# Optimization experiments

Measured on AMD Instinct MI355X. Metric: run time of the kernel, lower is better.

## Reference

```python
import jax, jax.numpy as jnp
import numpy as np

N_NODES = 100000
N_EDGES = 800000
NUM_GRAPHS = 512
IN_DIM = 16
EDGE_DIM = 1
HID = 64       # emb_dim
MLP_H = 32     # hidden_layers inside each MPNNLayer
L = 3          # num_layers
EPS = 1e-5


def setup_inputs() -> dict:
    key = jax.random.key(0)
    ks = jax.random.split(key, 24)
    s = 0.05
    inp = {
        "x": jax.random.normal(ks[0], (N_NODES, IN_DIM), jnp.float32),
        "edge_index": jax.random.randint(ks[1], (2, N_EDGES), 0, N_NODES),
        "edge_attr": jax.random.uniform(ks[2], (N_EDGES, EDGE_DIM), jnp.float32),
        "batch": jnp.sort(jax.random.randint(ks[3], (N_NODES,), 0, NUM_GRAPHS)),
        # input projection
        "lin_in_w": jax.random.normal(ks[4], (IN_DIM, HID), jnp.float32) * s,
        "lin_in_b": jnp.zeros((HID,), jnp.float32),
        # message MLP (stacked over L layers): Linear(129->32), BN(32), ReLU, Linear(32->64), ReLU, BN(64)
        "msg_w1": jax.random.normal(ks[5], (L, 2 * HID + EDGE_DIM, MLP_H), jnp.float32) * s,
        "msg_b1": jnp.zeros((L, MLP_H), jnp.float32),
        "msg_g1": jnp.ones((L, MLP_H), jnp.float32),
        "msg_be1": jnp.zeros((L, MLP_H), jnp.float32),
        "msg_w2": jax.random.normal(ks[6], (L, MLP_H, HID), jnp.float32) * s,
        "msg_b2": jnp.zeros((L, HID), jnp.float32),
        "msg_g2": jnp.ones((L, HID), jnp.float32),
        "msg_be2": jnp.zeros((L, HID), jnp.float32),
        # update MLP: Linear(128->32), BN(32), ReLU, Linear(32->64), ReLU, BN(64)
        "upd_w1": jax.random.normal(ks[7], (L, 2 * HID, MLP_H), jnp.float32) * s,
        "upd_b1": jnp.zeros((L, MLP_H), jnp.float32),
        "upd_g1": jnp.ones((L, MLP_H), jnp.float32),
        "upd_be1": jnp.zeros((L, MLP_H), jnp.float32),
        "upd_w2": jax.random.normal(ks[8], (L, MLP_H, HID), jnp.float32) * s,
        "upd_b2": jnp.zeros((L, HID), jnp.float32),
        "upd_g2": jnp.ones((L, HID), jnp.float32),
        "upd_be2": jnp.zeros((L, HID), jnp.float32),
        # head Linear(64->1) + ReLU
        "out_w": jax.random.normal(ks[9], (HID, 1), jnp.float32) * s,
        "out_b": jnp.zeros((1,), jnp.float32),
    }
    return inp


def _bn(h, g, b):
    # BatchNorm1d, training-mode batch stats (biased variance), dropout treated as identity (eval)
    mu = jnp.mean(h, axis=0)
    var = jnp.var(h, axis=0)
    return g * (h - mu) * jax.lax.rsqrt(var + EPS) + b


def reference(x, edge_index, edge_attr, batch,
              lin_in_w, lin_in_b,
              msg_w1, msg_b1, msg_g1, msg_be1, msg_w2, msg_b2, msg_g2, msg_be2,
              upd_w1, upd_b1, upd_g1, upd_be1, upd_w2, upd_b2, upd_g2, upd_be2,
              out_w, out_b):
    src = edge_index[0]  # x_j source
    dst = edge_index[1]  # x_i target / aggregation index
    h = x @ lin_in_w + lin_in_b  # [N, HID]
    for l in range(L):
        # message: cat([x_i, x_j, edge_attr]) -> Linear -> BN -> ReLU -> Linear -> ReLU -> BN
        m_in = jnp.concatenate([h[dst], h[src], edge_attr], axis=1)  # [E, 2*HID+EDGE_DIM]
        m = jax.nn.relu(_bn(m_in @ msg_w1[l] + msg_b1[l], msg_g1[l], msg_be1[l]))
        m = _bn(jax.nn.relu(m @ msg_w2[l] + msg_b2[l]), msg_g2[l], msg_be2[l])
        # aggregate: scatter-add over destination nodes
        agg = jax.ops.segment_sum(m, dst, num_segments=N_NODES)  # [N, HID]
        # update: cat([x, aggr]) -> Linear -> BN -> ReLU -> Linear -> ReLU -> BN
        u_in = jnp.concatenate([h, agg], axis=1)  # [N, 2*HID]
        u = jax.nn.relu(_bn(u_in @ upd_w1[l] + upd_b1[l], upd_g1[l], upd_be1[l]))
        u = _bn(jax.nn.relu(u @ upd_w2[l] + upd_b2[l]), upd_g2[l], upd_be2[l])
        h = h + u  # residual (x += conv(...))
    # global mean pool
    pooled = jax.ops.segment_sum(h, batch, num_segments=NUM_GRAPHS)
    counts = jax.ops.segment_sum(jnp.ones((h.shape[0],), h.dtype), batch, num_segments=NUM_GRAPHS)
    pooled = pooled / jnp.maximum(counts, 1.0)[:, None]
    return jax.nn.relu(pooled @ out_w + out_b).reshape(-1)  # [NUM_GRAPHS]
```

## Files before the change

kernel.cpp:

```cpp
#include <hip/hip_runtime.h>
#include <hip/hip_bf16.h>

#define N_NODES   100000
#define N_EDGES   800000
#define NUM_GRAPHS 512
#define IN_DIM    16
#define HID       64
#define MLP_H     32
#define EPS       1e-5f
#define TPB       256
#define SCAN_B    1024
#define NCHUNK    ((N_NODES + SCAN_B - 1) / SCAN_B)
#define GSB       2048
#define NWAVES    (GSB * 4)
#define PER_W     ((N_EDGES + NWAVES - 1) / NWAVES)
#define NODEBLKS  ((N_NODES + 63) / 64)

using nh2   = decltype(__builtin_amdgcn_cvt_pkrtz(0.f, 0.f));
typedef _Float16 f16x8 __attribute__((ext_vector_type(8)));
typedef float    f32x4 __attribute__((ext_vector_type(4)));
typedef int      i32x4 __attribute__((ext_vector_type(4)));

__device__ __forceinline__ nh2 pack2(float a, float b) {
  return __builtin_amdgcn_cvt_pkrtz(a, b);
}
__device__ __forceinline__ float wsum(float v) {
  v += __shfl_xor(v, 1, 64);
  v += __shfl_xor(v, 2, 64);
  v += __shfl_xor(v, 4, 64);
  v += __shfl_xor(v, 8, 64);
  v += __shfl_xor(v, 16, 64);
  v += __shfl_xor(v, 32, 64);
  return v;
}
__device__ __forceinline__ int lbound(const int* __restrict__ rs, int key) {
  int lo = 0, hi = N_NODES;
  while (lo < hi) { int m = (lo + hi) >> 1; if (rs[m] < key) lo = m + 1; else hi = m; }
  return lo;
}

__global__ __launch_bounds__(TPB) void k_deg(const int* __restrict__ ei, int* __restrict__ deg) {
  int e = blockIdx.x * TPB + threadIdx.x;
  if (e < N_EDGES) atomicAdd(&deg[ei[N_EDGES + e]], 1);
}

__global__ __launch_bounds__(SCAN_B) void k_scan_part(const int* __restrict__ deg,
                                                      int* __restrict__ partials) {
  __shared__ int red[SCAN_B];
  int i = blockIdx.x * SCAN_B + threadIdx.x;
  red[threadIdx.x] = (i < N_NODES) ? deg[i] : 0;
  __syncthreads();
  for (int off = SCAN_B / 2; off > 0; off >>= 1) {
    if (threadIdx.x < off) red[threadIdx.x] += red[threadIdx.x + off];
    __syncthreads();
  }
  if (threadIdx.x == 0) partials[blockIdx.x] = red[0];
}

__global__ void k_scan_mid(int* __restrict__ partials, int* __restrict__ row_start) {
  int run = 0;
  for (int b = 0; b < NCHUNK; ++b) { int t = partials[b]; partials[b] = run; run += t; }
  row_start[N_NODES] = run;
}

__global__ __launch_bounds__(SCAN_B) void k_scan_fin(const int* __restrict__ deg,
                                                     const int* __restrict__ partials,
                                                     int* __restrict__ row_start,
                                                     int* __restrict__ cursor) {
  __shared__ int buf[2][SCAN_B];
  int t = threadIdx.x, i = blockIdx.x * SCAN_B + t;
  int v = (i < N_NODES) ? deg[i] : 0;
  buf[0][t] = v;
  __syncthreads();
  int cur = 0;
  for (int off = 1; off < SCAN_B; off <<= 1) {
    int nv = buf[cur][t] + ((t >= off) ? buf[cur][t - off] : 0);
    buf[cur ^ 1][t] = nv; cur ^= 1;
    __syncthreads();
  }
  if (i < N_NODES) {
    int excl = buf[cur][t] - v + partials[blockIdx.x];
    row_start[i] = excl;
    cursor[i] = excl;
  }
}

__global__ __launch_bounds__(TPB) void k_fill(const int* __restrict__ ei,
                                              const float* __restrict__ ea,
                                              int* __restrict__ cursor,
                                              i32x4* __restrict__ erec) {
  int e = blockIdx.x * TPB + threadIdx.x;
  if (e >= N_EDGES) return;
  int dst = ei[N_EDGES + e];
  int pos = atomicAdd(&cursor[dst], 1);
  i32x4 rec;
  rec[0] = ei[e];
  rec[1] = dst;
  rec[2] = __float_as_int(ea[e]);
  rec[3] = 0;
  erec[pos] = rec;
}

__global__ __launch_bounds__(TPB) void k_lin_in(const float* __restrict__ x,
                                                const float* __restrict__ w,
                                                const float* __restrict__ b,
                                                float* __restrict__ h) {
  int i = blockIdx.x * TPB + threadIdx.x;
  if (i >= N_NODES) return;
  float xi[IN_DIM];
  const float4* xp = reinterpret_cast<const float4*>(x + i * IN_DIM);
#pragma unroll
  for (int q = 0; q < 4; ++q) {
    float4 v = xp[q];
    xi[4*q] = v.x; xi[4*q+1] = v.y; xi[4*q+2] = v.z; xi[4*q+3] = v.w;
  }
  float4* hp = reinterpret_cast<float4*>(h + i * HID);
#pragma unroll
  for (int j4 = 0; j4 < HID/4; ++j4) {
    float o[4];
#pragma unroll
    for (int c = 0; c < 4; ++c) {
      int j = j4*4 + c;
      float acc = b[j];
#pragma unroll
      for (int k = 0; k < IN_DIM; ++k) acc += xi[k] * w[k*HID + j];
      o[c] = acc;
    }
    float4 ov = {o[0], o[1], o[2], o[3]};
    hp[j4] = ov;
  }
}

__global__ __launch_bounds__(TPB) void k_pq(const float* __restrict__ h,
                                            const float* __restrict__ w1,
                                            const float* __restrict__ b1,
                                            float* __restrict__ P,
                                            _Float16* __restrict__ Qh) {
  const int part = __builtin_amdgcn_readfirstlane(threadIdx.x >> 6);
  const int lane = threadIdx.x & 63;
  const int i = blockIdx.x * 64 + lane;
  if (i >= N_NODES) return;
  const int jb = (part & 1) * 16;
  const bool isQ = part >= 2;
  const float* wbase = w1 + (isQ ? 64 * MLP_H : 0) + jb;
  float acc[16];
#pragma unroll
  for (int j = 0; j < 16; ++j) acc[j] = isQ ? 0.f : b1[jb + j];
  const float4* hp = reinterpret_cast<const float4*>(h + i * HID);
#pragma unroll 4
  for (int k4 = 0; k4 < 16; ++k4) {
    float4 a = hp[k4];
    const float* wr = wbase + (k4*4) * MLP_H;
#pragma unroll
    for (int j = 0; j < 16; ++j)
      acc[j] += a.x*wr[j] + a.y*wr[MLP_H+j] + a.z*wr[2*MLP_H+j] + a.w*wr[3*MLP_H+j];
  }
  if (!isQ) {
    float4* pp = reinterpret_cast<float4*>(P + i * MLP_H + jb);
#pragma unroll
    for (int c = 0; c < 4; ++c) {
      float4 o = {acc[4*c], acc[4*c+1], acc[4*c+2], acc[4*c+3]};
      pp[c] = o;
    }
  } else {
    i32x4 o0, o1;
#pragma unroll
    for (int c = 0; c < 4; ++c) {
      o0[c] = __builtin_bit_cast(int, pack2(acc[2*c],     acc[2*c+1]));
      o1[c] = __builtin_bit_cast(int, pack2(acc[8+2*c],   acc[8+2*c+1]));
    }
    i32x4* qp = reinterpret_cast<i32x4*>(Qh + i * MLP_H + jb);
    qp[0] = o0; qp[1] = o1;
  }
}

__global__ __launch_bounds__(TPB) void k_gather(const float* __restrict__ P,
                                                const _Float16* __restrict__ Qh,
                                                const i32x4* __restrict__ erec,
                                                const float* __restrict__ w1,
                                                float* __restrict__ gstat) {
  const int lane = threadIdx.x & 63;
  const int fg   = lane & 3;
  const int sl   = lane >> 2;
  const int fb   = fg * 8;
  float wk[8];
#pragma unroll
  for (int i = 0; i < 8; ++i) wk[i] = w1[128 * MLP_H + fb + i];
  float sv[8], qs[8];
#pragma unroll
  for (int i = 0; i < 8; ++i) { sv[i] = 0.f; qs[i] = 0.f; }
  const int wv = blockIdx.x * 4 + (threadIdx.x >> 6);
  const int c0 = wv * PER_W;
  const int c1 = min(c0 + PER_W, N_EDGES);
  if (c0 < N_EDGES) {
    const int c1m1 = c1 - 1;
    const int rounds = (c1 - c0 + 15) >> 4;
#define EIDX(R) min(c0 + 16*(R) + sl, c1m1)
    i32x4 recA = erec[EIDX(0)];
    i32x4 recB = erec[EIDX(1)];
    i32x4 recH = erec[EIDX(2)];
    f16x8 qA  = *reinterpret_cast<const f16x8*>(Qh + recA[0] * MLP_H + fb);
    f32x4 pA0 = *reinterpret_cast<const f32x4*>(P + recA[1] * MLP_H + fb);
    f32x4 pA1 = *reinterpret_cast<const f32x4*>(P + recA[1] * MLP_H + fb + 4);
    float aA  = __int_as_float(recA[2]);
    f16x8 qB  = *reinterpret_cast<const f16x8*>(Qh + recB[0] * MLP_H + fb);
    f32x4 pB0 = *reinterpret_cast<const f32x4*>(P + recB[1] * MLP_H + fb);
    f32x4 pB1 = *reinterpret_cast<const f32x4*>(P + recB[1] * MLP_H + fb + 4);
    float aB  = __int_as_float(recB[2]);
    for (int r = 0; r < rounds; ++r) {
      i32x4 recN = erec[EIDX(r + 3)];
      f16x8 qC  = *reinterpret_cast<const f16x8*>(Qh + recH[0] * MLP_H + fb);
      f32x4 pC0 = *reinterpret_cast<const f32x4*>(P + recH[1] * MLP_H + fb);
      f32x4 pC1 = *reinterpret_cast<const f32x4*>(P + recH[1] * MLP_H + fb + 4);
      float aC  = __int_as_float(recH[2]);
      const bool vc = (c0 + 16*r + sl) < c1;
      if (vc) {
#pragma unroll
        for (int i = 0; i < 8; ++i) {
          float pv = (i < 4) ? pA0[i] : pA1[i - 4];
          float z = fmaf(aA, wk[i], pv) + (float)qA[i];
          sv[i] += z; qs[i] = fmaf(z, z, qs[i]);
        }
      }
      qA = qB; pA0 = pB0; pA1 = pB1; aA = aB;
      qB = qC; pB0 = pC0; pB1 = pC1; aB = aC;
      recH = recN;
    }
#undef EIDX
  }
#pragma unroll
  for (int i = 0; i < 8; ++i) {
    sv[i] += __shfl_xor(sv[i], 4, 64);  sv[i] += __shfl_xor(sv[i], 8, 64);
    sv[i] += __shfl_xor(sv[i], 16, 64); sv[i] += __shfl_xor(sv[i], 32, 64);
    qs[i] += __shfl_xor(qs[i], 4, 64);  qs[i] += __shfl_xor(qs[i], 8, 64);
    qs[i] += __shfl_xor(qs[i], 16, 64); qs[i] += __shfl_xor(qs[i], 32, 64);
  }
  __shared__ float ls[4][MLP_H], lq[4][MLP_H];
  const int w = threadIdx.x >> 6;
  if (lane < 4) {
#pragma unroll
    for (int i = 0; i < 8; ++i) { ls[w][fb + i] = sv[i]; lq[w][fb + i] = qs[i]; }
  }
  __syncthreads();
  const int t = threadIdx.x;
  if (t < MLP_H)
    unsafeAtomicAdd(&gstat[t], ls[0][t] + ls[1][t] + ls[2][t] + ls[3][t]);
  else if (t < 2*MLP_H)
    unsafeAtomicAdd(&gstat[t], lq[0][t-MLP_H] + lq[1][t-MLP_H] + lq[2][t-MLP_H] + lq[3][t-MLP_H]);
}

__global__ __launch_bounds__(TPB) void k_msgdot(const i32x4* __restrict__ erec,
                                                const _Float16* __restrict__ Qh,
                                                const float* __restrict__ P,
                                                const int* __restrict__ rs,
                                                const float* __restrict__ gstat_in,
                                                const float* __restrict__ g1,
                                                const float* __restrict__ be1,
                                                const float* __restrict__ w1,
                                                const float* __restrict__ w2,
                                                const float* __restrict__ b2,
                                                float* __restrict__ agg,
                                                float* __restrict__ gstat_out) {
  const int lane = threadIdx.x & 63;
  const int col = lane & 15;
  const int g   = lane >> 4;
  float a1v[8], c1v[8], aw[8];
#pragma unroll
  for (int i = 0; i < 8; ++i) {
    int kf = g*8 + i;
    float mu = gstat_in[kf] * (1.f / N_EDGES);
    float var = fmaxf(gstat_in[MLP_H + kf] * (1.f / N_EDGES) - mu * mu, 0.f);
    float a = g1[kf] * rsqrtf(var + EPS);
    a1v[i] = a; c1v[i] = be1[kf] - a * mu;
    aw[i] = a * w1[128 * MLP_H + kf];
  }
  f16x8 bf0, bf1, bf2, bf3;
#define MKB(BF, C) { i32x4 bw; \
  _Pragma("unroll") for (int ii = 0; ii < 4; ++ii) { \
    nh2 p = pack2(w2[(g*8 + 2*ii) * HID + (C)*16 + col], \
                  w2[(g*8 + 2*ii + 1) * HID + (C)*16 + col]); \
    bw[ii] = __builtin_bit_cast(int, p); } \
  BF = __builtin_bit_cast(f16x8, bw); }
  MKB(bf0, 0) MKB(bf1, 1) MKB(bf2, 2) MKB(bf3, 3)
#undef MKB
  float b2c[4];
#pragma unroll
  for (int c = 0; c < 4; ++c) b2c[c] = b2[c*16 + col];

  float sacc[4] = {0.f,0.f,0.f,0.f}, qacc[4] = {0.f,0.f,0.f,0.f};
  const int wv = blockIdx.x * 4 + (threadIdx.x >> 6);
  const int key0 = min(wv * PER_W, N_EDGES);
  const int key1 = min((wv + 1) * PER_W, N_EDGES);
  const int n0 = lbound(rs, key0);
  const int n1 = (wv == NWAVES - 1) ? N_NODES : lbound(rs, key1);

  if (n0 < n1) {
    const int eLast = rs[n1] - 1;
    i32x4 rec = erec[min(rs[n0] + col, eLast)];
    f16x8 qv = *reinterpret_cast<const f16x8*>(Qh + rec[0] * MLP_H + g * 8);
    for (int n = n0; n < n1; ++n) {
      const int start = rs[n], end = rs[n + 1];
      f32x4 p0 = *reinterpret_cast<const f32x4*>(P + n * MLP_H + g * 8);
      f32x4 p1 = *reinterpret_cast<const f32x4*>(P + n * MLP_H + g * 8 + 4);
      float pb[8];
#pragma unroll
      for (int i = 0; i < 8; ++i)
        pb[i] = fmaf(a1v[i], (i < 4) ? p0[i] : p1[i - 4], c1v[i]);
      float aggacc[4] = {0.f,0.f,0.f,0.f};
      for (int t0 = start; t0 < end; t0 += 16) {
        const int bnext = (t0 + 16 < end) ? (t0 + 16) : end;
        i32x4 recN = erec[min(bnext + col, eLast)];
        const float ea = __int_as_float(rec[2]);
        i32x4 awb;
#pragma unroll
        for (int i = 0; i < 4; ++i) {
          float m0 = fmaxf(fmaf(a1v[2*i],   (float)qv[2*i],   fmaf(ea, aw[2*i],   pb[2*i])),   0.f);
          float m1 = fmaxf(fmaf(a1v[2*i+1], (float)qv[2*i+1], fmaf(ea, aw[2*i+1], pb[2*i+1])), 0.f);
          awb[i] = __builtin_bit_cast(int, pack2(m0, m1));
        }
        f16x8 af = __builtin_bit_cast(f16x8, awb);
        f32x4 zc = {0.f,0.f,0.f,0.f};
        f32x4 cc0 = __builtin_amdgcn_mfma_f32_16x16x32_f16(af, bf0, zc, 0, 0, 0);
        f32x4 cc1 = __builtin_amdgcn_mfma_f32_16x16x32_f16(af, bf1, zc, 0, 0, 0);
        f32x4 cc2 = __builtin_amdgcn_mfma_f32_16x16x32_f16(af, bf2, zc, 0, 0, 0);
        f32x4 cc3 = __builtin_amdgcn_mfma_f32_16x16x32_f16(af, bf3, zc, 0, 0, 0);
        f16x8 qvN = *reinterpret_cast<const f16x8*>(Qh + recN[0] * MLP_H + g * 8);
        bool vld[4];
#pragma unroll
        for (int reg = 0; reg < 4; ++reg) vld[reg] = (t0 + g*4 + reg) < end;
#define EPI(CC, CI) { \
  _Pragma("unroll") for (int reg = 0; reg < 4; ++reg) { \
    float tv = fmaxf(CC[reg] + b2c[CI], 0.f); \
    tv = vld[reg] ? tv : 0.f; \
    aggacc[CI] += tv; qacc[CI] = fmaf(tv, tv, qacc[CI]); } }
        EPI(cc0, 0) EPI(cc1, 1) EPI(cc2, 2) EPI(cc3, 3)
#undef EPI
        rec = recN; qv = qvN;
      }
#pragma unroll
      for (int c = 0; c < 4; ++c) sacc[c] += aggacc[c];
#pragma unroll
      for (int c = 0; c < 4; ++c) {
        aggacc[c] += __shfl_xor(aggacc[c], 16, 64);
        aggacc[c] += __shfl_xor(aggacc[c], 32, 64);
      }
      float aout = (g == 0) ? aggacc[0] : (g == 1) ? aggacc[1] : (g == 2) ? aggacc[2] : aggacc[3];
      agg[n * HID + g * 16 + col] = aout;
    }
  }
#pragma unroll
  for (int c = 0; c < 4; ++c) {
    sacc[c] += __shfl_xor(sacc[c], 16, 64);
    sacc[c] += __shfl_xor(sacc[c], 32, 64);
    qacc[c] += __shfl_xor(qacc[c], 16, 64);
    qacc[c] += __shfl_xor(qacc[c], 32, 64);
  }
  __shared__ float ls[4][HID], lq[4][HID];
  const int w = threadIdx.x >> 6;
  if (g == 0) {
#pragma unroll
    for (int c = 0; c < 4; ++c) { ls[w][c*16 + col] = sacc[c]; lq[w][c*16 + col] = qacc[c]; }
  }
  __syncthreads();
  const int t = threadIdx.x;
  if (t < HID)
    unsafeAtomicAdd(&gstat_out[t], ls[0][t] + ls[1][t] + ls[2][t] + ls[3][t]);
  else if (t < 2*HID)
    unsafeAtomicAdd(&gstat_out[t], lq[0][t-HID] + lq[1][t-HID] + lq[2][t-HID] + lq[3][t-HID]);
}

__global__ __launch_bounds__(TPB) void k_upd1(const float* __restrict__ h,
                                              const float* __restrict__ agg,
                                              const int* __restrict__ deg,
                                              const float* __restrict__ gstat_in,
                                              const float* __restrict__ g2,
                                              const float* __restrict__ be2,
                                              const float* __restrict__ w1,
                                              const float* __restrict__ b1,
                                              float* __restrict__ zu1) {
  __shared__ float sa[HID], sc[HID];
  {
    int t = threadIdx.x;
    if (t < HID) {
      float mu = gstat_in[t] * (1.f / N_EDGES);
      float var = fmaxf(gstat_in[HID + t] * (1.f / N_EDGES) - mu * mu, 0.f);
      float a = g2[t] * rsqrtf(var + EPS);
      sa[t] = a; sc[t] = be2[t] - a * mu;
    }
  }
  __syncthreads();
  const int widx = __builtin_amdgcn_readfirstlane(threadIdx.x >> 6);
  const int part = widx & 1;
  const int grp  = blockIdx.x * 2 + (widx >> 1);
  const int lane = threadIdx.x & 63;
  const int jb = part * 16;
  const int i = grp * 64 + lane;
  if (i >= N_NODES) return;
  float acc[16];
#pragma unroll
  for (int j = 0; j < 16; ++j) acc[j] = b1[jb + j];
  const float4* hp = reinterpret_cast<const float4*>(h + i * HID);
#pragma unroll 4
  for (int k4 = 0; k4 < 16; ++k4) {
    float4 a = hp[k4];
    const float* wr = w1 + (k4*4) * MLP_H + jb;
#pragma unroll
    for (int j = 0; j < 16; ++j)
      acc[j] += a.x*wr[j] + a.y*wr[MLP_H+j] + a.z*wr[2*MLP_H+j] + a.w*wr[3*MLP_H+j];
  }
  float degf = (float)deg[i];
  const float4* ap = reinterpret_cast<const float4*>(agg + i * HID);
#pragma unroll 4
  for (int k4 = 0; k4 < 16; ++k4) {
    float4 g4 = ap[k4];
    int k = k4*4;
    float a0 = sa[k]  *g4.x + sc[k]  *degf;
    float a1 = sa[k+1]*g4.y + sc[k+1]*degf;
    float a2 = sa[k+2]*g4.z + sc[k+2]*degf;
    float a3 = sa[k+3]*g4.w + sc[k+3]*degf;
    const float* wr = w1 + (64 + k) * MLP_H + jb;
#pragma unroll
    for (int j = 0; j < 16; ++j)
      acc[j] += a0*wr[j] + a1*wr[MLP_H+j] + a2*wr[2*MLP_H+j] + a3*wr[3*MLP_H+j];
  }
  float4* zp = reinterpret_cast<float4*>(zu1 + i * MLP_H + jb);
#pragma unroll
  for (int c = 0; c < 4; ++c) {
    float4 o = {acc[4*c], acc[4*c+1], acc[4*c+2], acc[4*c+3]};
    zp[c] = o;
  }
}

__global__ __launch_bounds__(TPB) void k_upd2(const float* __restrict__ zu1,
                                              const float* __restrict__ gstat_in,
                                              const float* __restrict__ gu1,
                                              const float* __restrict__ beu1,
                                              const float* __restrict__ w2,
                                              const float* __restrict__ b2,
                                              float* __restrict__ tu) {
  __shared__ float sa[MLP_H], sc[MLP_H];
  {
    int t = threadIdx.x;
    if (t < MLP_H) {
      float mu = gstat_in[t] * (1.f / N_NODES);
      float var = fmaxf(gstat_in[MLP_H + t] * (1.f / N_NODES) - mu * mu, 0.f);
      float a = gu1[t] * rsqrtf(var + EPS);
      sa[t] = a; sc[t] = beu1[t] - a * mu;
    }
  }
  __syncthreads();
  const int widx = __builtin_amdgcn_readfirstlane(threadIdx.x >> 6);
  const int part = widx & 1;
  const int grp  = blockIdx.x * 2 + (widx >> 1);
  const int lane = threadIdx.x & 63;
  const int jb = part * 32;
  const int i = grp * 64 + lane;
  if (i >= N_NODES) return;
  float m1[MLP_H];
  const float4* zp = reinterpret_cast<const float4*>(zu1 + i * MLP_H);
#pragma unroll
  for (int c = 0; c < MLP_H/4; ++c) {
    float4 z = zp[c];
    int kk = 4*c;
    m1[kk]   = fmaxf(sa[kk]  *z.x + sc[kk],   0.f);
    m1[kk+1] = fmaxf(sa[kk+1]*z.y + sc[kk+1], 0.f);
    m1[kk+2] = fmaxf(sa[kk+2]*z.z + sc[kk+2], 0.f);
    m1[kk+3] = fmaxf(sa[kk+3]*z.w + sc[kk+3], 0.f);
  }
#pragma unroll
  for (int j4 = 0; j4 < 8; ++j4) {
    float tv[4];
#pragma unroll
    for (int c = 0; c < 4; ++c) {
      int j = jb + j4*4 + c;
      float v = b2[j];
#pragma unroll
      for (int kk = 0; kk < MLP_H; ++kk) v += m1[kk] * w2[kk*HID + j];
      tv[c] = fmaxf(v, 0.f);
    }
    float4 o = {tv[0], tv[1], tv[2], tv[3]};
    *reinterpret_cast<float4*>(tu + i * HID + jb + j4*4) = o;
  }
}

template <int NF>
__global__ __launch_bounds__(TPB) void k_colstats(const float* __restrict__ X,
                                                  int nrows, float* __restrict__ gstat) {
  const int RPB = TPB / NF;
  int f = threadIdx.x % NF;
  int rloc = threadIdx.x / NF;
  float s = 0.f, q = 0.f;
  for (int r = blockIdx.x * RPB + rloc; r < nrows; r += gridDim.x * RPB) {
    float v = X[r * NF + f];
    s += v; q = fmaf(v, v, q);
  }
  __shared__ float ls[TPB], lq[TPB];
  ls[threadIdx.x] = s; lq[threadIdx.x] = q;
  __syncthreads();
  if (threadIdx.x < NF) {
    float ss = 0.f, qq = 0.f;
#pragma unroll
    for (int r = 0; r < RPB; ++r) { ss += ls[r*NF + f]; qq += lq[r*NF + f]; }
    unsafeAtomicAdd(&gstat[f], ss);
    unsafeAtomicAdd(&gstat[NF + f], qq);
  }
}

__global__ __launch_bounds__(TPB) void k_resid(float* __restrict__ h,
                                               const float* __restrict__ tu,
                                               const float* __restrict__ gstat_in,
                                               const float* __restrict__ gu2,
                                               const float* __restrict__ beu2) {
  __shared__ float sa[HID], sc[HID];
  {
    int t = threadIdx.x;
    if (t < HID) {
      float mu = gstat_in[t] * (1.f / N_NODES);
      float var = fmaxf(gstat_in[HID + t] * (1.f / N_NODES) - mu * mu, 0.f);
      float a = gu2[t] * rsqrtf(var + EPS);
      sa[t] = a; sc[t] = beu2[t] - a * mu;
    }
  }
  __syncthreads();
  int idx = blockIdx.x * TPB + threadIdx.x;
  if (idx >= N_NODES * (HID/4)) return;
  int j0 = (idx & (HID/4 - 1)) * 4;
  float4 hv = reinterpret_cast<const float4*>(h)[idx];
  float4 tv = reinterpret_cast<const float4*>(tu)[idx];
  hv.x += sa[j0]  *tv.x + sc[j0];
  hv.y += sa[j0+1]*tv.y + sc[j0+1];
  hv.z += sa[j0+2]*tv.z + sc[j0+2];
  hv.w += sa[j0+3]*tv.w + sc[j0+3];
  reinterpret_cast<float4*>(h)[idx] = hv;
}

__global__ __launch_bounds__(TPB) void k_pool_head(const float* __restrict__ h,
                                                   const int* __restrict__ batch,
                                                   const float* __restrict__ ow,
                                                   const float* __restrict__ ob,
                                                   float* __restrict__ out) {
  int g = blockIdx.x;
  int lo = 0, hi = N_NODES;
  while (lo < hi) { int mid = (lo+hi) >> 1; if (batch[mid] < g) lo = mid+1; else hi = mid; }
  int start = lo;
  lo = start; hi = N_NODES;
  while (lo < hi) { int mid = (lo+hi) >> 1; if (batch[mid] < g+1) lo = mid+1; else hi = mid; }
  int end = lo;
  int j = threadIdx.x & 63;
  int sub = threadIdx.x >> 6;
  float acc = 0.f;
  for (int n = start + sub; n < end; n += 4) acc += h[n*HID + j];
  __shared__ float red[TPB];
  red[threadIdx.x] = acc;
  __syncthreads();
  if (threadIdx.x < 64) {
    float s = red[threadIdx.x] + red[64+threadIdx.x] + red[128+threadIdx.x] + red[192+threadIdx.x];
    float cnt = (float)(end - start);
    float pooled = s / fmaxf(cnt, 1.0f);
    float v = pooled * ow[threadIdx.x];
    v = wsum(v);
    if (threadIdx.x == 0) out[g] = fmaxf(v + ob[0], 0.f);
  }
}

extern "C" void kernel_launch(void* const* d_in, const int* in_sizes, int n_in,
                              void* d_out, int out_size, void* d_ws, size_t ws_size,
                              hipStream_t stream) {
  const float* x       = (const float*)d_in[0];
  const int*   ei      = (const int*)  d_in[1];
  const float* ea      = (const float*)d_in[2];
  const int*   batch   = (const int*)  d_in[3];
  const float* lin_w   = (const float*)d_in[4];
  const float* lin_b   = (const float*)d_in[5];
  const float* msg_w1  = (const float*)d_in[6];
  const float* msg_b1  = (const float*)d_in[7];
  const float* msg_g1  = (const float*)d_in[8];
  const float* msg_be1 = (const float*)d_in[9];
  const float* msg_w2  = (const float*)d_in[10];
  const float* msg_b2  = (const float*)d_in[11];
  const float* msg_g2  = (const float*)d_in[12];
  const float* msg_be2 = (const float*)d_in[13];
  const float* upd_w1  = (const float*)d_in[14];
  const float* upd_b1  = (const float*)d_in[15];
  const float* upd_g1  = (const float*)d_in[16];
  const float* upd_be1 = (const float*)d_in[17];
  const float* upd_w2  = (const float*)d_in[18];
  const float* upd_b2  = (const float*)d_in[19];
  const float* upd_g2  = (const float*)d_in[20];
  const float* upd_be2 = (const float*)d_in[21];
  const float* out_w   = (const float*)d_in[22];
  const float* out_b   = (const float*)d_in[23];
  float* out = (float*)d_out;

  float* W     = (float*)d_ws;
  float* h     = W;
  float* P     = W + 6400000;
  _Float16* Qh = (_Float16*)(W + 9600000);
  float* agg   = W + 12800000;
  float* zu1   = W + 32000000;
  float* tu    = W + 35200000;
  float* stats = W + 41600000;
  int*   ib    = (int*)(W + 41601152);
  int* deg       = ib;
  int* row_start = ib + 100000;
  int* cursor    = ib + 200001;
  int* partials  = ib + 300001;
  i32x4* erec    = (i32x4*)(ib + 300232);

  hipMemsetAsync(stats, 0, 3*384*sizeof(float), stream);
  hipMemsetAsync(deg, 0, N_NODES*sizeof(int), stream);

  k_deg<<<N_EDGES/TPB, TPB, 0, stream>>>(ei, deg);
  k_scan_part<<<NCHUNK, SCAN_B, 0, stream>>>(deg, partials);
  k_scan_mid<<<1, 1, 0, stream>>>(partials, row_start);
  k_scan_fin<<<NCHUNK, SCAN_B, 0, stream>>>(deg, partials, row_start, cursor);
  k_fill<<<N_EDGES/TPB, TPB, 0, stream>>>(ei, ea, cursor, erec);

  k_lin_in<<<(N_NODES+TPB-1)/TPB, TPB, 0, stream>>>(x, lin_w, lin_b, h);

  const int PQ_BLKS   = NODEBLKS;
  const int UPD_BLKS  = (NODEBLKS + 1) / 2;

  for (int l = 0; l < 3; ++l) {
    const float* mw1 = msg_w1 + (size_t)l*129*MLP_H;
    const float* mb1 = msg_b1 + l*MLP_H;
    const float* mg1 = msg_g1 + l*MLP_H;
    const float* mbe1= msg_be1 + l*MLP_H;
    const float* mw2 = msg_w2 + (size_t)l*MLP_H*HID;
    const float* mb2 = msg_b2 + l*HID;
    const float* mg2 = msg_g2 + l*HID;
    const float* mbe2= msg_be2 + l*HID;
    const float* uw1 = upd_w1 + (size_t)l*128*MLP_H;
    const float* ub1 = upd_b1 + l*MLP_H;
    const float* ug1 = upd_g1 + l*MLP_H;
    const float* ube1= upd_be1 + l*MLP_H;
    const float* uw2 = upd_w2 + (size_t)l*MLP_H*HID;
    const float* ub2 = upd_b2 + l*HID;
    const float* ug2 = upd_g2 + l*HID;
    const float* ube2= upd_be2 + l*HID;
    float* st = stats + l*384;

    k_pq<<<PQ_BLKS, TPB, 0, stream>>>(h, mw1, mb1, P, Qh);
    k_gather<<<GSB, TPB, 0, stream>>>(P, Qh, erec, mw1, st);
    k_msgdot<<<GSB, TPB, 0, stream>>>(erec, Qh, P, row_start, st, mg1, mbe1, mw1, mw2, mb2,
                                      agg, st+64);
    k_upd1<<<UPD_BLKS, TPB, 0, stream>>>(h, agg, deg, st+64, mg2, mbe2, uw1, ub1, zu1);
    k_colstats<MLP_H><<<512, TPB, 0, stream>>>(zu1, N_NODES, st+192);
    k_upd2<<<UPD_BLKS, TPB, 0, stream>>>(zu1, st+192, ug1, ube1, uw2, ub2, tu);
    k_colstats<HID><<<512, TPB, 0, stream>>>(tu, N_NODES, st+256);
    k_resid<<<(N_NODES*(HID/4)+TPB-1)/TPB, TPB, 0, stream>>>(h, tu, st+256, ug2, ube2);
  }

  k_pool_head<<<NUM_GRAPHS, TPB, 0, stream>>>(h, batch, out_w, out_b, out);
}
```

Baseline: 1.005 ms.

## Pad CSR rows to groups of four and materialize first-layer activations in fp16

Each node's edge list is padded to a multiple of four, with dummy records flagged so they are left out of the BN statistics. The gather kernel now writes the first linear pre-activation per edge slot to an fp16 buffer. The message kernel then processes fixed 16-slot tiles with a node map instead of binary-searching node ranges, and accumulates into agg with float atomics, which requires a per-layer memset. This removes the per-node loop and its irregular work split, at the cost of an extra fp16 intermediate write and read, padding work, and atomic traffic.

```diff
diff --git a/kernel.cpp b/kernel.cpp
--- a/kernel.cpp
+++ b/kernel.cpp
@@ -13,7 +13,9 @@
 #define NCHUNK    ((N_NODES + SCAN_B - 1) / SCAN_B)
 #define GSB       2048
 #define NWAVES    (GSB * 4)
-#define PER_W     ((N_EDGES + NWAVES - 1) / NWAVES)
+#define EPAD_MAX  1100000
+#define PER_WP    ((EPAD_MAX + NWAVES - 1) / NWAVES)
+#define NMAP_MAX  (EPAD_MAX/4 + 8)
 #define NODEBLKS  ((N_NODES + 63) / 64)
 
 using nh2   = decltype(__builtin_amdgcn_cvt_pkrtz(0.f, 0.f));
@@ -33,11 +35,6 @@
   v += __shfl_xor(v, 32, 64);
   return v;
 }
-__device__ __forceinline__ int lbound(const int* __restrict__ rs, int key) {
-  int lo = 0, hi = N_NODES;
-  while (lo < hi) { int m = (lo + hi) >> 1; if (rs[m] < key) lo = m + 1; else hi = m; }
-  return lo;
-}
 
 __global__ __launch_bounds__(TPB) void k_deg(const int* __restrict__ ei, int* __restrict__ deg) {
   int e = blockIdx.x * TPB + threadIdx.x;
@@ -48,7 +45,7 @@
                                                       int* __restrict__ partials) {
   __shared__ int red[SCAN_B];
   int i = blockIdx.x * SCAN_B + threadIdx.x;
-  red[threadIdx.x] = (i < N_NODES) ? deg[i] : 0;
+  red[threadIdx.x] = (i < N_NODES) ? ((deg[i] + 3) & ~3) : 0;
   __syncthreads();
   for (int off = SCAN_B / 2; off > 0; off >>= 1) {
     if (threadIdx.x < off) red[threadIdx.x] += red[threadIdx.x + off];
@@ -57,19 +54,19 @@
   if (threadIdx.x == 0) partials[blockIdx.x] = red[0];
 }
 
-__global__ void k_scan_mid(int* __restrict__ partials, int* __restrict__ row_start) {
+__global__ void k_scan_mid(int* __restrict__ partials, int* __restrict__ rs_pad) {
   int run = 0;
   for (int b = 0; b < NCHUNK; ++b) { int t = partials[b]; partials[b] = run; run += t; }
-  row_start[N_NODES] = run;
+  rs_pad[N_NODES] = run;
 }
 
 __global__ __launch_bounds__(SCAN_B) void k_scan_fin(const int* __restrict__ deg,
                                                      const int* __restrict__ partials,
-                                                     int* __restrict__ row_start,
+                                                     int* __restrict__ rs_pad,
                                                      int* __restrict__ cursor) {
   __shared__ int buf[2][SCAN_B];
   int t = threadIdx.x, i = blockIdx.x * SCAN_B + t;
-  int v = (i < N_NODES) ? deg[i] : 0;
+  int v = (i < N_NODES) ? ((deg[i] + 3) & ~3) : 0;
   buf[0][t] = v;
   __syncthreads();
   int cur = 0;
@@ -80,7 +77,7 @@
   }
   if (i < N_NODES) {
     int excl = buf[cur][t] - v + partials[blockIdx.x];
-    row_start[i] = excl;
+    rs_pad[i] = excl;
     cursor[i] = excl;
   }
 }
@@ -97,8 +94,26 @@
   rec[0] = ei[e];
   rec[1] = dst;
   rec[2] = __float_as_int(ea[e]);
-  rec[3] = 0;
+  rec[3] = 1;
   erec[pos] = rec;
+}
+
+__global__ __launch_bounds__(TPB) void k_pad(const int* __restrict__ deg,
+                                             const int* __restrict__ rs_pad,
+                                             i32x4* __restrict__ erec,
+                                             int* __restrict__ nmap) {
+  int n = blockIdx.x * TPB + threadIdx.x;
+  if (n >= N_NODES) return;
+  int d = deg[n];
+  int ps = rs_pad[n];
+  int gcnt = (d + 3) >> 2;
+  for (int j = 0; j < gcnt; ++j) {
+    int vcnt = d - 4 * j; if (vcnt > 4) vcnt = 4;
+    nmap[(ps >> 2) + j] = n | (vcnt << 20);
+  }
+  int pd = gcnt * 4;
+  i32x4 rec; rec[0] = 0; rec[1] = n; rec[2] = 0; rec[3] = 0;
+  for (int s = d; s < pd; ++s) erec[ps + s] = rec;
 }
 
 __global__ __launch_bounds__(TPB) void k_lin_in(const float* __restrict__ x,
@@ -178,6 +193,8 @@
                                                 const _Float16* __restrict__ Qh,
                                                 const i32x4* __restrict__ erec,
                                                 const float* __restrict__ w1,
+                                                const int* __restrict__ rs_pad,
+                                                _Float16* __restrict__ z1h,
                                                 float* __restrict__ gstat) {
   const int lane = threadIdx.x & 63;
   const int fg   = lane & 3;
@@ -189,10 +206,11 @@
   float sv[8], qs[8];
 #pragma unroll
   for (int i = 0; i < 8; ++i) { sv[i] = 0.f; qs[i] = 0.f; }
+  const int Epad = rs_pad[N_NODES];
   const int wv = blockIdx.x * 4 + (threadIdx.x >> 6);
-  const int c0 = wv * PER_W;
-  const int c1 = min(c0 + PER_W, N_EDGES);
-  if (c0 < N_EDGES) {
+  const int c0 = wv * PER_WP;
+  const int c1 = min(c0 + PER_WP, Epad);
+  if (c0 < Epad) {
     const int c1m1 = c1 - 1;
     const int rounds = (c1 - c0 + 15) >> 4;
 #define EIDX(R) min(c0 + 16*(R) + sl, c1m1)
@@ -203,27 +221,40 @@
     f32x4 pA0 = *reinterpret_cast<const f32x4*>(P + recA[1] * MLP_H + fb);
     f32x4 pA1 = *reinterpret_cast<const f32x4*>(P + recA[1] * MLP_H + fb + 4);
     float aA  = __int_as_float(recA[2]);
+    int   fA  = recA[3];
     f16x8 qB  = *reinterpret_cast<const f16x8*>(Qh + recB[0] * MLP_H + fb);
     f32x4 pB0 = *reinterpret_cast<const f32x4*>(P + recB[1] * MLP_H + fb);
     f32x4 pB1 = *reinterpret_cast<const f32x4*>(P + recB[1] * MLP_H + fb + 4);
     float aB  = __int_as_float(recB[2]);
+    int   fB  = recB[3];
     for (int r = 0; r < rounds; ++r) {
       i32x4 recN = erec[EIDX(r + 3)];
       f16x8 qC  = *reinterpret_cast<const f16x8*>(Qh + recH[0] * MLP_H + fb);
       f32x4 pC0 = *reinterpret_cast<const f32x4*>(P + recH[1] * MLP_H + fb);
       f32x4 pC1 = *reinterpret_cast<const f32x4*>(P + recH[1] * MLP_H + fb + 4);
       float aC  = __int_as_float(recH[2]);
-      const bool vc = (c0 + 16*r + sl) < c1;
+      int   fC  = recH[3];
+      const int slot = c0 + 16*r + sl;
+      const bool vc = slot < c1;
+      float z[8];
+#pragma unroll
+      for (int i = 0; i < 8; ++i) {
+        float pv = (i < 4) ? pA0[i] : pA1[i - 4];
+        z[i] = fmaf(aA, wk[i], pv) + (float)qA[i];
+      }
       if (vc) {
-#pragma unroll
-        for (int i = 0; i < 8; ++i) {
-          float pv = (i < 4) ? pA0[i] : pA1[i - 4];
-          float z = fmaf(aA, wk[i], pv) + (float)qA[i];
-          sv[i] += z; qs[i] = fmaf(z, z, qs[i]);
+        i32x4 zp;
+#pragma unroll
+        for (int ii = 0; ii < 4; ++ii)
+          zp[ii] = __builtin_bit_cast(int, pack2(z[2*ii], z[2*ii+1]));
+        *reinterpret_cast<i32x4*>(z1h + slot * MLP_H + fb) = zp;
+        if (fA) {
+#pragma unroll
+          for (int i = 0; i < 8; ++i) { sv[i] += z[i]; qs[i] = fmaf(z[i], z[i], qs[i]); }
         }
       }
-      qA = qB; pA0 = pB0; pA1 = pB1; aA = aB;
-      qB = qC; pB0 = pC0; pB1 = pC1; aB = aC;
+      qA = qB; pA0 = pB0; pA1 = pB1; aA = aB; fA = fB;
+      qB = qC; pB0 = pC0; pB1 = pC1; aB = aC; fB = fC;
       recH = recN;
     }
 #undef EIDX
@@ -249,14 +280,12 @@
     unsafeAtomicAdd(&gstat[t], lq[0][t-MLP_H] + lq[1][t-MLP_H] + lq[2][t-MLP_H] + lq[3][t-MLP_H]);
 }
 
-__global__ __launch_bounds__(TPB) void k_msgdot(const i32x4* __restrict__ erec,
-                                                const _Float16* __restrict__ Qh,
-                                                const float* __restrict__ P,
-                                                const int* __restrict__ rs,
+__global__ __launch_bounds__(TPB) void k_msgdot(const _Float16* __restrict__ z1h,
+                                                const int* __restrict__ nmap,
+                                                const int* __restrict__ rs_pad,
                                                 const float* __restrict__ gstat_in,
                                                 const float* __restrict__ g1,
                                                 const float* __restrict__ be1,
-                                                const float* __restrict__ w1,
                                                 const float* __restrict__ w2,
                                                 const float* __restrict__ b2,
                                                 float* __restrict__ agg,
@@ -264,7 +293,7 @@
   const int lane = threadIdx.x & 63;
   const int col = lane & 15;
   const int g   = lane >> 4;
-  float a1v[8], c1v[8], aw[8];
+  float a1v[8], c1v[8];
 #pragma unroll
   for (int i = 0; i < 8; ++i) {
     int kf = g*8 + i;
@@ -272,7 +301,6 @@
     float var = fmaxf(gstat_in[MLP_H + kf] * (1.f / N_EDGES) - mu * mu, 0.f);
     float a = g1[kf] * rsqrtf(var + EPS);
     a1v[i] = a; c1v[i] = be1[kf] - a * mu;
-    aw[i] = a * w1[128 * MLP_H + kf];
   }
   f16x8 bf0, bf1, bf2, bf3;
 #define MKB(BF, C) { i32x4 bw; \
@@ -288,64 +316,51 @@
   for (int c = 0; c < 4; ++c) b2c[c] = b2[c*16 + col];
 
   float sacc[4] = {0.f,0.f,0.f,0.f}, qacc[4] = {0.f,0.f,0.f,0.f};
+  const int Epad = rs_pad[N_NODES];
+  const int ntiles = (Epad + 15) >> 4;
   const int wv = blockIdx.x * 4 + (threadIdx.x >> 6);
-  const int key0 = min(wv * PER_W, N_EDGES);
-  const int key1 = min((wv + 1) * PER_W, N_EDGES);
-  const int n0 = lbound(rs, key0);
-  const int n1 = (wv == NWAVES - 1) ? N_NODES : lbound(rs, key1);
-
-  if (n0 < n1) {
-    const int eLast = rs[n1] - 1;
-    i32x4 rec = erec[min(rs[n0] + col, eLast)];
-    f16x8 qv = *reinterpret_cast<const f16x8*>(Qh + rec[0] * MLP_H + g * 8);
-    for (int n = n0; n < n1; ++n) {
-      const int start = rs[n], end = rs[n + 1];
-      f32x4 p0 = *reinterpret_cast<const f32x4*>(P + n * MLP_H + g * 8);
-      f32x4 p1 = *reinterpret_cast<const f32x4*>(P + n * MLP_H + g * 8 + 4);
-      float pb[8];
-#pragma unroll
-      for (int i = 0; i < 8; ++i)
-        pb[i] = fmaf(a1v[i], (i < 4) ? p0[i] : p1[i - 4], c1v[i]);
-      float aggacc[4] = {0.f,0.f,0.f,0.f};
-      for (int t0 = start; t0 < end; t0 += 16) {
-        const int bnext = (t0 + 16 < end) ? (t0 + 16) : end;
-        i32x4 recN = erec[min(bnext + col, eLast)];
-        const float ea = __int_as_float(rec[2]);
-        i32x4 awb;
-#pragma unroll
-        for (int i = 0; i < 4; ++i) {
-          float m0 = fmaxf(fmaf(a1v[2*i],   (float)qv[2*i],   fmaf(ea, aw[2*i],   pb[2*i])),   0.f);
-          float m1 = fmaxf(fmaf(a1v[2*i+1], (float)qv[2*i+1], fmaf(ea, aw[2*i+1], pb[2*i+1])), 0.f);
-          awb[i] = __builtin_bit_cast(int, pack2(m0, m1));
-        }
-        f16x8 af = __builtin_bit_cast(f16x8, awb);
-        f32x4 zc = {0.f,0.f,0.f,0.f};
-        f32x4 cc0 = __builtin_amdgcn_mfma_f32_16x16x32_f16(af, bf0, zc, 0, 0, 0);
-        f32x4 cc1 = __builtin_amdgcn_mfma_f32_16x16x32_f16(af, bf1, zc, 0, 0, 0);
-        f32x4 cc2 = __builtin_amdgcn_mfma_f32_16x16x32_f16(af, bf2, zc, 0, 0, 0);
-        f32x4 cc3 = __builtin_amdgcn_mfma_f32_16x16x32_f16(af, bf3, zc, 0, 0, 0);
-        f16x8 qvN = *reinterpret_cast<const f16x8*>(Qh + recN[0] * MLP_H + g * 8);
-        bool vld[4];
-#pragma unroll
-        for (int reg = 0; reg < 4; ++reg) vld[reg] = (t0 + g*4 + reg) < end;
+
+  if (wv < ntiles) {
+    int tile = wv;
+    int t0 = tile * 16;
+    f16x8 zv = *reinterpret_cast<const f16x8*>(z1h + (t0 + col) * MLP_H + g * 8);
+    int nm = nmap[(t0 >> 2) + g];
+    while (true) {
+      const int tileN = tile + NWAVES;
+      const bool hasN = tileN < ntiles;
+      const int tN = hasN ? tileN * 16 : t0;
+      f16x8 zvN = *reinterpret_cast<const f16x8*>(z1h + (tN + col) * MLP_H + g * 8);
+      int nmN = nmap[(tN >> 2) + g];
+      i32x4 aw;
+#pragma unroll
+      for (int i = 0; i < 4; ++i) {
+        float m0 = fmaxf(fmaf(a1v[2*i],   (float)zv[2*i],   c1v[2*i]),   0.f);
+        float m1 = fmaxf(fmaf(a1v[2*i+1], (float)zv[2*i+1], c1v[2*i+1]), 0.f);
+        aw[i] = __builtin_bit_cast(int, pack2(m0, m1));
+      }
+      f16x8 af = __builtin_bit_cast(f16x8, aw);
+      f32x4 zc = {0.f,0.f,0.f,0.f};
+      f32x4 cc0 = __builtin_amdgcn_mfma_f32_16x16x32_f16(af, bf0, zc, 0, 0, 0);
+      f32x4 cc1 = __builtin_amdgcn_mfma_f32_16x16x32_f16(af, bf1, zc, 0, 0, 0);
+      f32x4 cc2 = __builtin_amdgcn_mfma_f32_16x16x32_f16(af, bf2, zc, 0, 0, 0);
+      f32x4 cc3 = __builtin_amdgcn_mfma_f32_16x16x32_f16(af, bf3, zc, 0, 0, 0);
+      const int nid = nm & 0xFFFFF;
+      const int vcnt = (nm >> 20) & 7;
+      bool vld[4];
+#pragma unroll
+      for (int reg = 0; reg < 4; ++reg) vld[reg] = reg < vcnt;
 #define EPI(CC, CI) { \
-  _Pragma("unroll") for (int reg = 0; reg < 4; ++reg) { \
-    float tv = fmaxf(CC[reg] + b2c[CI], 0.f); \
-    tv = vld[reg] ? tv : 0.f; \
-    aggacc[CI] += tv; qacc[CI] = fmaf(tv, tv, qacc[CI]); } }
-        EPI(cc0, 0) EPI(cc1, 1) EPI(cc2, 2) EPI(cc3, 3)
+    float s4 = 0.f; \
+    _Pragma("unroll") for (int reg = 0; reg < 4; ++reg) { \
+      float tv = fmaxf(CC[reg] + b2c[CI], 0.f); \
+      tv = vld[reg] ? tv : 0.f; \
+      s4 += tv; qacc[CI] = fmaf(tv, tv, qacc[CI]); } \
+    sacc[CI] += s4; \
+    unsafeAtomicAdd(&agg[nid * HID + (CI)*16 + col], s4); }
+      EPI(cc0, 0) EPI(cc1, 1) EPI(cc2, 2) EPI(cc3, 3)
 #undef EPI
-        rec = recN; qv = qvN;
-      }
-#pragma unroll
-      for (int c = 0; c < 4; ++c) sacc[c] += aggacc[c];
-#pragma unroll
-      for (int c = 0; c < 4; ++c) {
-        aggacc[c] += __shfl_xor(aggacc[c], 16, 64);
-        aggacc[c] += __shfl_xor(aggacc[c], 32, 64);
-      }
-      float aout = (g == 0) ? aggacc[0] : (g == 1) ? aggacc[1] : (g == 2) ? aggacc[2] : aggacc[3];
-      agg[n * HID + g * 16 + col] = aout;
+      if (!hasN) break;
+      tile = tileN; t0 = tN; zv = zvN; nm = nmN;
     }
   }
 #pragma unroll
@@ -596,30 +611,34 @@
   float* h     = W;
   float* P     = W + 6400000;
   _Float16* Qh = (_Float16*)(W + 9600000);
-  float* agg   = W + 12800000;
-  float* zu1   = W + 32000000;
-  float* tu    = W + 35200000;
-  float* stats = W + 41600000;
-  int*   ib    = (int*)(W + 41601152);
+  float* agg   = W + 11200000;
+  _Float16* z1h = (_Float16*)(W + 17600000);
+  float* zu1   = W + 17600000;
+  float* tu    = W + 20800000;
+  float* stats = W + 35200512;
+  int*   ib    = (int*)(W + 35201664);
   int* deg       = ib;
-  int* row_start = ib + 100000;
+  int* rs_pad    = ib + 100000;
   int* cursor    = ib + 200001;
   int* partials  = ib + 300001;
-  i32x4* erec    = (i32x4*)(ib + 300232);
+  int* nmap      = ib + 300136;
+  i32x4* erec    = (i32x4*)(ib + 575148);
 
   hipMemsetAsync(stats, 0, 3*384*sizeof(float), stream);
   hipMemsetAsync(deg, 0, N_NODES*sizeof(int), stream);
+  hipMemsetAsync(nmap, 0, NMAP_MAX*sizeof(int), stream);
 
   k_deg<<<N_EDGES/TPB, TPB, 0, stream>>>(ei, deg);
   k_scan_part<<<NCHUNK, SCAN_B, 0, stream>>>(deg, partials);
-  k_scan_mid<<<1, 1, 0, stream>>>(partials, row_start);
-  k_scan_fin<<<NCHUNK, SCAN_B, 0, stream>>>(deg, partials, row_start, cursor);
+  k_scan_mid<<<1, 1, 0, stream>>>(partials, rs_pad);
+  k_scan_fin<<<NCHUNK, SCAN_B, 0, stream>>>(deg, partials, rs_pad, cursor);
   k_fill<<<N_EDGES/TPB, TPB, 0, stream>>>(ei, ea, cursor, erec);
+  k_pad<<<(N_NODES+TPB-1)/TPB, TPB, 0, stream>>>(deg, rs_pad, erec, nmap);
 
   k_lin_in<<<(N_NODES+TPB-1)/TPB, TPB, 0, stream>>>(x, lin_w, lin_b, h);
 
-  const int PQ_BLKS   = NODEBLKS;
-  const int UPD_BLKS  = (NODEBLKS + 1) / 2;
+  const int PQ_BLKS  = NODEBLKS;
+  const int UPD_BLKS = (NODEBLKS + 1) / 2;
 
   for (int l = 0; l < 3; ++l) {
     const float* mw1 = msg_w1 + (size_t)l*129*MLP_H;
@@ -640,9 +659,10 @@
     const float* ube2= upd_be2 + l*HID;
     float* st = stats + l*384;
 
+    hipMemsetAsync(agg, 0, (size_t)N_NODES*HID*sizeof(float), stream);
     k_pq<<<PQ_BLKS, TPB, 0, stream>>>(h, mw1, mb1, P, Qh);
-    k_gather<<<GSB, TPB, 0, stream>>>(P, Qh, erec, mw1, st);
-    k_msgdot<<<GSB, TPB, 0, stream>>>(erec, Qh, P, row_start, st, mg1, mbe1, mw1, mw2, mb2,
+    k_gather<<<GSB, TPB, 0, stream>>>(P, Qh, erec, mw1, rs_pad, z1h, st);
+    k_msgdot<<<GSB, TPB, 0, stream>>>(z1h, nmap, rs_pad, st, mg1, mbe1, mw2, mb2,
                                       agg, st+64);
     k_upd1<<<UPD_BLKS, TPB, 0, stream>>>(h, agg, deg, st+64, mg2, mbe2, uw1, ub1, zu1);
     k_colstats<MLP_H><<<512, TPB, 0, stream>>>(zu1, N_NODES, st+192);
```

After: 1.225 ms. 21.9% more time.
